# Kernel tuning notes

Measured on AMD Instinct MI355X. Metric: run time of the kernel, lower is better.

The kernel has to match this reference:

```python
import jax, jax.numpy as jnp
import numpy as np

B, N, D, H = 4, 16384, 64, 8
MIN_FREQ = 1.0 / 64.0
SCALE = 1.0
EPS = 1e-5


def layernorm(x):
    # LayerNorm over last (head-feature) dim, no affine, biased variance (torch default)
    m = jnp.mean(x, axis=-1, keepdims=True)
    v = jnp.mean(jnp.square(x - m), axis=-1, keepdims=True)
    return (x - m) * jax.lax.rsqrt(v + EPS)


def rope_freqs(pos):
    # pos: [b, n, 1] 1-D coordinates -> freqs [b, n, D]
    inv_freq = 1.0 / (10000.0 ** (jnp.arange(0, D, 2, dtype=jnp.float32) / D))  # [D/2]
    t = pos[..., 0] * (SCALE / MIN_FREQ)                                         # [b, n]
    f = t[..., None] * inv_freq                                                  # [b, n, D/2]
    return jnp.concatenate([f, f], axis=-1)                                      # [b, n, D]


def rotate_half(x):
    x1, x2 = jnp.split(x, 2, axis=-1)
    return jnp.concatenate([-x2, x1], axis=-1)


def apply_rope(x, freqs):
    # x: [b, h, n, d], freqs: [b, n, d]
    c = jnp.cos(freqs)[:, None]
    s = jnp.sin(freqs)[:, None]
    return x * c + rotate_half(x) * s


def setup_inputs() -> dict:
    key = jax.random.key(0)
    ks = jax.random.split(key, 6)
    gain = 1.0 / D
    return {
        "x": jax.random.normal(ks[0], (B, N, D), dtype=jnp.float32),
        "pos": jax.random.uniform(ks[1], (B, N, 1), dtype=jnp.float32),
        "Wq": jax.random.normal(ks[2], (D, D * H), dtype=jnp.float32) * gain,
        "Wk": jax.random.normal(ks[3], (D, D * H), dtype=jnp.float32) * gain,
        "Wv": jax.random.normal(ks[4], (D, D * H), dtype=jnp.float32) * gain,
        "Wo": jax.random.normal(ks[5], (D * H, D), dtype=jnp.float32) * gain,
    }


def reference(x, pos, Wq, Wk, Wv, Wo):
    b, n, _ = x.shape

    def proj(W):
        # [b, n, d] @ [d, h*d] -> [b, h, n, d]
        y = jnp.einsum("bnd,de->bne", x, W)
        return y.reshape(b, n, H, D).transpose(0, 2, 1, 3)

    q, k, v = proj(Wq), proj(Wk), proj(Wv)

    # galerkin: layernorm k and v (no mask path)
    k = layernorm(k)
    v = layernorm(v)

    # RoPE on q, k
    freqs = rope_freqs(pos)
    q = apply_rope(q, freqs)
    k = apply_rope(k, freqs)

    # linear attention: z = q @ (k^T v) / n
    kv = jnp.einsum("bhnd,bhne->bhde", k, v)          # [b, h, d, d]
    z = jnp.einsum("bhnd,bhde->bhne", q, kv) / n      # [b, h, n, d]
    z = z.transpose(0, 2, 1, 3).reshape(b, n, H * D)  # [b, n, h*d]

    return jnp.einsum("bne,ed->bnd", z, Wo)           # out_proj (dropout=0)
```

## Files before the change

kernel.cpp:

```cpp
#include <hip/hip_runtime.h>

#define B_ 4
#define N_ 16384
#define D_ 64
#define H_ 8
#define E_ 512
#define NCHUNK 16
#define NTILES (N_ / 64)

typedef __attribute__((ext_vector_type(8))) short short8;
typedef __attribute__((ext_vector_type(4))) float f32x4;
typedef __attribute__((ext_vector_type(2))) unsigned int uint32x2;

__device__ __forceinline__ unsigned short f2b(float f) {
    unsigned u = __float_as_uint(f);
    return (unsigned short)((u + 0x7fffu + ((u >> 16) & 1u)) >> 16);
}

__device__ __forceinline__ unsigned cvtpk(float a, float b) {
    unsigned r;
    asm("v_cvt_pk_bf16_f32 %0, %1, %2" : "=v"(r) : "v"(a), "v"(b));
    return r;
}

template<int CTRL>
__device__ __forceinline__ float dppadd(float x) {
    int y = __builtin_amdgcn_update_dpp(0, __float_as_int(x), CTRL, 0xF, 0xF, true);
    return x + __int_as_float(y);
}
__device__ __forceinline__ float rowsum16(float x) {
    x = dppadd<0xB1>(x);
    x = dppadd<0x4E>(x);
    x = dppadd<0x141>(x);
    x = dppadd<0x140>(x);
    return x;
}

__global__ __launch_bounds__(256) void k_prep(
    const float* __restrict__ x,
    const float* __restrict__ Wq, const float* __restrict__ Wk,
    const float* __restrict__ Wv,
    unsigned short* __restrict__ WqB, unsigned short* __restrict__ WkB,
    unsigned short* __restrict__ WvB,
    unsigned short* __restrict__ xblob)
{
    const int bid = blockIdx.x, tid = threadIdx.x;
    if (bid < 384) {
        int mat = bid >> 7, sub = bid & 127;
        const float* src = (mat == 0) ? Wq : (mat == 1) ? Wk : Wv;
        unsigned short* dst = (mat == 0) ? WqB : (mat == 1) ? WkB : WvB;
        int id = sub * 256 + tid;
        int kin = id >> 9, f = id & 511;
        int h = f >> 6, feat = f & 63;
        int nt = feat >> 4, cc = feat & 15;
        int half = kin >> 5, qd = (kin >> 3) & 3, e = kin & 7;
        dst[(size_t)h * 4096 + (((nt * 2 + half) * 64 + qd * 16 + cc) * 8) + e]
            = f2b(src[id]);
        return;
    }
    int idx = (bid - 384) * 256 + tid;
    int lane = idx & 63, fr = (idx >> 6) & 1, tb = (idx >> 7) & 1023, b = idx >> 17;
    int cc = lane & 15, qd = lane >> 4;
    const float* src = &x[((size_t)b * N_ + tb * 16 + cc) * 64 + fr * 32 + qd * 8];
    float4 v0 = *(const float4*)src;
    float4 v1 = *(const float4*)(src + 4);
    ushort4 u0, u1;
    u0.x = f2b(v0.x); u0.y = f2b(v0.y); u0.z = f2b(v0.z); u0.w = f2b(v0.w);
    u1.x = f2b(v1.x); u1.y = f2b(v1.y); u1.z = f2b(v1.z); u1.w = f2b(v1.w);
    *(ushort4*)&xblob[(size_t)idx * 8]     = u0;
    *(ushort4*)&xblob[(size_t)idx * 8 + 4] = u1;
}

__global__ __launch_bounds__(256, 2) void k_kv(
    const unsigned short* __restrict__ xblob,
    const float* __restrict__ pos,
    const unsigned short* __restrict__ WkB,
    const unsigned short* __restrict__ WvB,
    float* __restrict__ kv_part)
{
    const int b = blockIdx.z, h = blockIdx.y, chunk = blockIdx.x;
    const int tid  = threadIdx.x;
    const int lane = tid & 63;
    const int w    = tid >> 6;
    const int c    = lane & 15;
    const int quad = lane >> 4;
    const int m0   = w * 16;

    __shared__ unsigned short kbuf[2][64 * 72];
    __shared__ unsigned short vbuf[2][64 * 72];

    short8 WK[8], WV[8];
    {
        const unsigned short* wk0 = WkB + (size_t)h * 4096 + (size_t)lane * 8;
        const unsigned short* wv0 = WvB + (size_t)h * 4096 + (size_t)lane * 8;
        #pragma unroll
        for (int fr = 0; fr < 8; ++fr) WK[fr] = *(const short8*)&wk0[fr * 512];
        #pragma unroll
        for (int fr = 0; fr < 8; ++fr) WV[fr] = *(const short8*)&wv0[fr * 512];
    }
    __builtin_amdgcn_sched_barrier(0);

    const float invf_lo = exp2f(-0.4152410118609203f * (float)c);
    const float invf_hi = invf_lo * 0.01f;

    f32x4 akv[4];
    #pragma unroll
    for (int nt = 0; nt < 4; ++nt) akv[nt] = (f32x4){0.f, 0.f, 0.f, 0.f};

    short8 a0, a1;
    float tp[4];
    {
        int tb = chunk * 4 + w;
        const unsigned short* xb = xblob + (size_t)((b * 1024 + tb) * 2) * 512 + lane * 8;
        a0 = *(const short8*)&xb[0];
        a1 = *(const short8*)&xb[512];
        #pragma unroll
        for (int r = 0; r < 4; ++r)
            tp[r] = pos[(size_t)b * N_ + chunk * 64 + m0 + quad * 4 + r] * 64.0f;
    }

    int p = 0;
    for (int tile = chunk; tile < NTILES; tile += NCHUNK) {
        f32x4 ak[4], av[4];
        #pragma unroll
        for (int nt = 0; nt < 4; ++nt) {
            f32x4 z = {0.f, 0.f, 0.f, 0.f};
            z = __builtin_amdgcn_mfma_f32_16x16x32_bf16(a0, WK[nt * 2 + 0], z, 0, 0, 0);
            ak[nt] = __builtin_amdgcn_mfma_f32_16x16x32_bf16(a1, WK[nt * 2 + 1], z, 0, 0, 0);
            f32x4 y = {0.f, 0.f, 0.f, 0.f};
            y = __builtin_amdgcn_mfma_f32_16x16x32_bf16(a0, WV[nt * 2 + 0], y, 0, 0, 0);
            av[nt] = __builtin_amdgcn_mfma_f32_16x16x32_bf16(a1, WV[nt * 2 + 1], y, 0, 0, 0);
        }

        float cl[4], sl[4], ch[4], sh[4];
        #pragma unroll
        for (int r = 0; r < 4; ++r) {
            float al = tp[r] * invf_lo, ah = tp[r] * invf_hi;
            cl[r] = __cosf(al); sl[r] = __sinf(al);
            ch[r] = __cosf(ah); sh[r] = __sinf(ah);
        }

        const int tn = tile + NCHUNK;
        if (tn < NTILES) {
            int tb = tn * 4 + w;
            const unsigned short* xb = xblob + (size_t)((b * 1024 + tb) * 2) * 512 + lane * 8;
            a0 = *(const short8*)&xb[0];
            a1 = *(const short8*)&xb[512];
            #pragma unroll
            for (int r = 0; r < 4; ++r)
                tp[r] = pos[(size_t)b * N_ + tn * 64 + m0 + quad * 4 + r] * 64.0f;
        }
        __builtin_amdgcn_sched_barrier(0);

        #pragma unroll
        for (int r = 0; r < 4; ++r) {
            float sk  = ak[0][r] + ak[1][r] + ak[2][r] + ak[3][r];
            float sk2 = ak[0][r]*ak[0][r] + ak[1][r]*ak[1][r] + ak[2][r]*ak[2][r] + ak[3][r]*ak[3][r];
            float sv  = av[0][r] + av[1][r] + av[2][r] + av[3][r];
            float sv2 = av[0][r]*av[0][r] + av[1][r]*av[1][r] + av[2][r]*av[2][r] + av[3][r]*av[3][r];
            sk = rowsum16(sk); sk2 = rowsum16(sk2);
            sv = rowsum16(sv); sv2 = rowsum16(sv2);
            float mk = sk * (1.0f / 64.0f);
            float rk = rsqrtf(sk2 * (1.0f / 64.0f) - mk * mk + 1e-5f);
            float mv = sv * (1.0f / 64.0f);
            float rv = rsqrtf(sv2 * (1.0f / 64.0f) - mv * mv + 1e-5f);
            #pragma unroll
            for (int nt = 0; nt < 4; ++nt) {
                ak[nt][r] = (ak[nt][r] - mk) * rk;
                av[nt][r] = (av[nt][r] - mv) * rv;
            }
        }

        #pragma unroll
        for (int r = 0; r < 4; ++r) {
            float lo0 = ak[0][r], hi0 = ak[2][r];
            ak[0][r] = lo0 * cl[r] - hi0 * sl[r];
            ak[2][r] = hi0 * cl[r] + lo0 * sl[r];
            float lo1 = ak[1][r], hi1 = ak[3][r];
            ak[1][r] = lo1 * ch[r] - hi1 * sh[r];
            ak[3][r] = hi1 * ch[r] + lo1 * sh[r];
        }

        #pragma unroll
        for (int nt = 0; nt < 4; ++nt) {
            uint32x2 kk, vv;
            kk[0] = cvtpk(ak[nt][0], ak[nt][1]);
            kk[1] = cvtpk(ak[nt][2], ak[nt][3]);
            vv[0] = cvtpk(av[nt][0], av[nt][1]);
            vv[1] = cvtpk(av[nt][2], av[nt][3]);
            *(uint32x2*)&kbuf[p][(nt * 16 + c) * 72 + m0 + quad * 4] = kk;
            *(uint32x2*)&vbuf[p][(nt * 16 + c) * 72 + m0 + quad * 4] = vv;
        }
        __syncthreads();

        short8 ka0 = *(const short8*)&kbuf[p][(m0 + c) * 72 + quad * 8];
        short8 ka1 = *(const short8*)&kbuf[p][(m0 + c) * 72 + 32 + quad * 8];
        #pragma unroll
        for (int nt = 0; nt < 4; ++nt) {
            short8 vb0 = *(const short8*)&vbuf[p][(nt * 16 + c) * 72 + quad * 8];
            short8 vb1 = *(const short8*)&vbuf[p][(nt * 16 + c) * 72 + 32 + quad * 8];
            akv[nt] = __builtin_amdgcn_mfma_f32_16x16x32_bf16(ka0, vb0, akv[nt], 0, 0, 0);
            akv[nt] = __builtin_amdgcn_mfma_f32_16x16x32_bf16(ka1, vb1, akv[nt], 0, 0, 0);
        }
        p ^= 1;
    }

    float* dst = kv_part + ((size_t)(b * H_ + h) * NCHUNK + chunk) * 4096;
    #pragma unroll
    for (int nt = 0; nt < 4; ++nt)
        #pragma unroll
        for (int r = 0; r < 4; ++r)
            dst[(size_t)(16 * w + quad * 4 + r) * 64 + nt * 16 + c] = akv[nt][r];
}

__global__ __launch_bounds__(256) void k_m(
    const float* __restrict__ kv_part,
    const float* __restrict__ Wo,
    unsigned short* __restrict__ MTB)
{
    const int h = blockIdx.x, b = blockIdx.y;
    const int tid = threadIdx.x;
    __shared__ float kvs[64 * 65];
    __shared__ float wos[64 * 68];

    const float* src = kv_part + (size_t)(b * H_ + h) * NCHUNK * 4096;
    for (int i = tid; i < 4096; i += 256) {
        float s = 0.f;
        #pragma unroll
        for (int ch = 0; ch < NCHUNK; ++ch) s += src[ch * 4096 + i];
        kvs[(i >> 6) * 65 + (i & 63)] = s;
    }
    for (int i = tid; i < 1024; i += 256) {
        int dp = i >> 4, j4 = (i & 15) * 4;
        *(float4*)&wos[dp * 68 + j4] = *(const float4*)&Wo[(size_t)(h * 64 + dp) * 64 + j4];
    }
    __syncthreads();

    const int j0 = (tid & 15) * 4, d0 = (tid >> 4) * 4;
    float acc[4][4] = {{0.f}};
    #pragma unroll 4
    for (int dp = 0; dp < 64; ++dp) {
        float a_[4];
        #pragma unroll
        for (int i = 0; i < 4; ++i) a_[i] = kvs[(d0 + i) * 65 + dp];
        float4 w4 = *(const float4*)&wos[dp * 68 + j0];
        float w_[4] = {w4.x, w4.y, w4.z, w4.w};
        #pragma unroll
        for (int i = 0; i < 4; ++i)
            #pragma unroll
            for (int j = 0; j < 4; ++j)
                acc[i][j] += a_[i] * w_[j];
    }
    const float inv_n = 1.0f / (float)N_;
    unsigned short* dst = MTB + (size_t)(b * H_ + h) * 4096;
    #pragma unroll
    for (int i = 0; i < 4; ++i)
        #pragma unroll
        for (int j = 0; j < 4; ++j) {
            int d = d0 + i, jj = j0 + j;
            int nt = jj >> 4, cc = jj & 15;
            int half = d >> 5, qd = (d >> 3) & 3, e = d & 7;
            dst[(((nt * 2 + half) * 64 + qd * 16 + cc) * 8) + e] = f2b(acc[i][j] * inv_n);
        }
}

__global__ __launch_bounds__(256, 2) void k_out(
    const unsigned short* __restrict__ xblob,
    const float* __restrict__ pos,
    const unsigned short* __restrict__ WqB,
    const unsigned short* __restrict__ MTB,
    float* __restrict__ out)
{
    const int b = blockIdx.y;
    const int n0 = blockIdx.x * 64;
    const int tid  = threadIdx.x;
    const int lane = tid & 63;
    const int w    = tid >> 6;
    const int c    = lane & 15;
    const int quad = lane >> 4;
    const int m0   = w * 16;

    __shared__ unsigned short qbuf[64 * 72];

    const int tb = blockIdx.x * 4 + w;
    const unsigned short* xb = xblob + (size_t)((b * 1024 + tb) * 2) * 512 + lane * 8;
    short8 a0 = *(const short8*)&xb[0];
    short8 a1 = *(const short8*)&xb[512];

    const unsigned short* wq0 = WqB + (size_t)lane * 8;
    const unsigned short* mt0 = MTB + (size_t)(b * H_) * 4096 + (size_t)lane * 8;
    short8 W[8], Mt[8];
    #pragma unroll
    for (int fr = 0; fr < 8; ++fr) W[fr]  = *(const short8*)&wq0[fr * 512];
    #pragma unroll
    for (int fr = 0; fr < 8; ++fr) Mt[fr] = *(const short8*)&mt0[fr * 512];
    __builtin_amdgcn_sched_barrier(0);

    const float invf_lo = exp2f(-0.4152410118609203f * (float)c);
    const float invf_hi = invf_lo * 0.01f;
    float csl[4], snl[4], csh[4], snh[4];
    #pragma unroll
    for (int r = 0; r < 4; ++r) {
        float tpv = pos[(size_t)b * N_ + n0 + m0 + quad * 4 + r] * 64.0f;
        float al = tpv * invf_lo, ah = tpv * invf_hi;
        csl[r] = __cosf(al); snl[r] = __sinf(al);
        csh[r] = __cosf(ah); snh[r] = __sinf(ah);
    }

    f32x4 oacc[4];
    #pragma unroll
    for (int nt = 0; nt < 4; ++nt) oacc[nt] = (f32x4){0.f, 0.f, 0.f, 0.f};

    #pragma unroll
    for (int h = 0; h < H_; ++h) {
        f32x4 aq[4];
        #pragma unroll
        for (int nt = 0; nt < 4; ++nt) {
            f32x4 z = {0.f, 0.f, 0.f, 0.f};
            z = __builtin_amdgcn_mfma_f32_16x16x32_bf16(a0, W[nt * 2 + 0], z, 0, 0, 0);
            aq[nt] = __builtin_amdgcn_mfma_f32_16x16x32_bf16(a1, W[nt * 2 + 1], z, 0, 0, 0);
        }

        if (h < H_ - 1) {
            #pragma unroll
            for (int fr = 0; fr < 8; ++fr)
                W[fr] = *(const short8*)&wq0[(size_t)(h + 1) * 4096 + fr * 512];
        }
        __builtin_amdgcn_sched_barrier(0);

        #pragma unroll
        for (int r = 0; r < 4; ++r) {
            float lo0 = aq[0][r], hi0 = aq[2][r];
            aq[0][r] = lo0 * csl[r] - hi0 * snl[r];
            aq[2][r] = hi0 * csl[r] + lo0 * snl[r];
            float lo1 = aq[1][r], hi1 = aq[3][r];
            aq[1][r] = lo1 * csh[r] - hi1 * snh[r];
            aq[3][r] = hi1 * csh[r] + lo1 * snh[r];
        }

        #pragma unroll
        for (int nt = 0; nt < 4; ++nt) {
            unsigned q01 = cvtpk(aq[nt][0], aq[nt][1]);
            unsigned q23 = cvtpk(aq[nt][2], aq[nt][3]);
            int base = (m0 + quad * 4) * 72 + nt * 16 + c;
            qbuf[base]       = (unsigned short)q01;
            qbuf[base + 72]  = (unsigned short)(q01 >> 16);
            qbuf[base + 144] = (unsigned short)q23;
            qbuf[base + 216] = (unsigned short)(q23 >> 16);
        }

        short8 qa0 = *(const short8*)&qbuf[(m0 + c) * 72 + quad * 8];
        short8 qa1 = *(const short8*)&qbuf[(m0 + c) * 72 + 32 + quad * 8];
        #pragma unroll
        for (int nt = 0; nt < 4; ++nt) {
            oacc[nt] = __builtin_amdgcn_mfma_f32_16x16x32_bf16(qa0, Mt[nt * 2 + 0], oacc[nt], 0, 0, 0);
            oacc[nt] = __builtin_amdgcn_mfma_f32_16x16x32_bf16(qa1, Mt[nt * 2 + 1], oacc[nt], 0, 0, 0);
        }

        if (h < H_ - 1) {
            #pragma unroll
            for (int fr = 0; fr < 8; ++fr)
                Mt[fr] = *(const short8*)&mt0[(size_t)(h + 1) * 4096 + fr * 512];
        }
        __builtin_amdgcn_sched_barrier(0);
    }

    #pragma unroll
    for (int nt = 0; nt < 4; ++nt)
        #pragma unroll
        for (int r = 0; r < 4; ++r)
            out[(size_t)(b * N_ + n0 + m0 + quad * 4 + r) * 64 + nt * 16 + c] = oacc[nt][r];
}

extern "C" void kernel_launch(void* const* d_in, const int* in_sizes, int n_in,
                              void* d_out, int out_size, void* d_ws, size_t ws_size,
                              hipStream_t stream)
{
    const float* x   = (const float*)d_in[0];
    const float* pos = (const float*)d_in[1];
    const float* Wq  = (const float*)d_in[2];
    const float* Wk  = (const float*)d_in[3];
    const float* Wv  = (const float*)d_in[4];
    const float* Wo  = (const float*)d_in[5];
    float* out = (float*)d_out;

    char* ws = (char*)d_ws;
    float* kv_part        = (float*)ws;
    unsigned short* MTB   = (unsigned short*)(ws + 8388608);
    unsigned short* WqB   = (unsigned short*)(ws + 8650752);
    unsigned short* WkB   = (unsigned short*)(ws + 8716288);
    unsigned short* WvB   = (unsigned short*)(ws + 8781824);
    unsigned short* xblob = (unsigned short*)(ws + 8847360);

    k_prep<<<dim3(2432), 256, 0, stream>>>(x, Wq, Wk, Wv,
                                           WqB, WkB, WvB, xblob);
    k_kv  <<<dim3(NCHUNK, H_, B_), 256, 0, stream>>>(xblob, pos, WkB, WvB, kv_part);
    k_m   <<<dim3(H_, B_), 256, 0, stream>>>(kv_part, Wo, MTB);
    k_out <<<dim3(NTILES, B_), 256, 0, stream>>>(xblob, pos, WqB, MTB, out);
}
```

Before: 151.2 us.

## Double k_kv chunk count and process two 64-row tiles per k_out block

Raises k_kv parallelism from 16 to 32 chunks per (b,h) with a higher occupancy hint, and moves the workspace offsets to fit the larger partial buffer. k_out now handles 128 rows per block, so each Wq/Mt weight fragment loaded into registers is reused across two row tiles, halving the weight reloads and the block count. The cost is more register pressure in k_out, a larger kv_part reduction in k_m, and fewer k_out blocks to fill the GPU.

```diff
diff --git a/kernel.cpp b/kernel.cpp
--- a/kernel.cpp
+++ b/kernel.cpp
@@ -5,7 +5,7 @@
 #define D_ 64
 #define H_ 8
 #define E_ 512
-#define NCHUNK 16
+#define NCHUNK 32
 #define NTILES (N_ / 64)
 
 typedef __attribute__((ext_vector_type(8))) short short8;
@@ -71,7 +71,7 @@
     *(ushort4*)&xblob[(size_t)idx * 8 + 4] = u1;
 }
 
-__global__ __launch_bounds__(256, 2) void k_kv(
+__global__ __launch_bounds__(256, 4) void k_kv(
     const unsigned short* __restrict__ xblob,
     const float* __restrict__ pos,
     const unsigned short* __restrict__ WkB,
@@ -226,7 +226,7 @@
     const float* src = kv_part + (size_t)(b * H_ + h) * NCHUNK * 4096;
     for (int i = tid; i < 4096; i += 256) {
         float s = 0.f;
-        #pragma unroll
+        #pragma unroll 8
         for (int ch = 0; ch < NCHUNK; ++ch) s += src[ch * 4096 + i];
         kvs[(i >> 6) * 65 + (i & 63)] = s;
     }
@@ -272,7 +272,7 @@
     float* __restrict__ out)
 {
     const int b = blockIdx.y;
-    const int n0 = blockIdx.x * 64;
+    const int n0 = blockIdx.x * 128;
     const int tid  = threadIdx.x;
     const int lane = tid & 63;
     const int w    = tid >> 6;
@@ -280,12 +280,16 @@
     const int quad = lane >> 4;
     const int m0   = w * 16;
 
-    __shared__ unsigned short qbuf[64 * 72];
-
-    const int tb = blockIdx.x * 4 + w;
-    const unsigned short* xb = xblob + (size_t)((b * 1024 + tb) * 2) * 512 + lane * 8;
-    short8 a0 = *(const short8*)&xb[0];
-    short8 a1 = *(const short8*)&xb[512];
+    __shared__ unsigned short qbuf[128 * 72];
+
+    const int tbA = blockIdx.x * 8 + w;
+    const int tbB = blockIdx.x * 8 + 4 + w;
+    const unsigned short* xbA = xblob + (size_t)((b * 1024 + tbA) * 2) * 512 + lane * 8;
+    const unsigned short* xbB = xblob + (size_t)((b * 1024 + tbB) * 2) * 512 + lane * 8;
+    short8 aA0 = *(const short8*)&xbA[0];
+    short8 aA1 = *(const short8*)&xbA[512];
+    short8 aB0 = *(const short8*)&xbB[0];
+    short8 aB1 = *(const short8*)&xbB[512];
 
     const unsigned short* wq0 = WqB + (size_t)lane * 8;
     const unsigned short* mt0 = MTB + (size_t)(b * H_) * 4096 + (size_t)lane * 8;
@@ -298,27 +302,38 @@
 
     const float invf_lo = exp2f(-0.4152410118609203f * (float)c);
     const float invf_hi = invf_lo * 0.01f;
-    float csl[4], snl[4], csh[4], snh[4];
+    float cslA[4], snlA[4], cshA[4], snhA[4];
+    float cslB[4], snlB[4], cshB[4], snhB[4];
     #pragma unroll
     for (int r = 0; r < 4; ++r) {
-        float tpv = pos[(size_t)b * N_ + n0 + m0 + quad * 4 + r] * 64.0f;
-        float al = tpv * invf_lo, ah = tpv * invf_hi;
-        csl[r] = __cosf(al); snl[r] = __sinf(al);
-        csh[r] = __cosf(ah); snh[r] = __sinf(ah);
-    }
-
-    f32x4 oacc[4];
-    #pragma unroll
-    for (int nt = 0; nt < 4; ++nt) oacc[nt] = (f32x4){0.f, 0.f, 0.f, 0.f};
+        float tA = pos[(size_t)b * N_ + n0 + m0 + quad * 4 + r] * 64.0f;
+        float aAl = tA * invf_lo, aAh = tA * invf_hi;
+        cslA[r] = __cosf(aAl); snlA[r] = __sinf(aAl);
+        cshA[r] = __cosf(aAh); snhA[r] = __sinf(aAh);
+        float tB = pos[(size_t)b * N_ + n0 + 64 + m0 + quad * 4 + r] * 64.0f;
+        float aBl = tB * invf_lo, aBh = tB * invf_hi;
+        cslB[r] = __cosf(aBl); snlB[r] = __sinf(aBl);
+        cshB[r] = __cosf(aBh); snhB[r] = __sinf(aBh);
+    }
+
+    f32x4 oaccA[4], oaccB[4];
+    #pragma unroll
+    for (int nt = 0; nt < 4; ++nt) {
+        oaccA[nt] = (f32x4){0.f, 0.f, 0.f, 0.f};
+        oaccB[nt] = (f32x4){0.f, 0.f, 0.f, 0.f};
+    }
 
     #pragma unroll
     for (int h = 0; h < H_; ++h) {
-        f32x4 aq[4];
+        f32x4 aqA[4], aqB[4];
         #pragma unroll
         for (int nt = 0; nt < 4; ++nt) {
             f32x4 z = {0.f, 0.f, 0.f, 0.f};
-            z = __builtin_amdgcn_mfma_f32_16x16x32_bf16(a0, W[nt * 2 + 0], z, 0, 0, 0);
-            aq[nt] = __builtin_amdgcn_mfma_f32_16x16x32_bf16(a1, W[nt * 2 + 1], z, 0, 0, 0);
+            z = __builtin_amdgcn_mfma_f32_16x16x32_bf16(aA0, W[nt * 2 + 0], z, 0, 0, 0);
+            aqA[nt] = __builtin_amdgcn_mfma_f32_16x16x32_bf16(aA1, W[nt * 2 + 1], z, 0, 0, 0);
+            f32x4 y = {0.f, 0.f, 0.f, 0.f};
+            y = __builtin_amdgcn_mfma_f32_16x16x32_bf16(aB0, W[nt * 2 + 0], y, 0, 0, 0);
+            aqB[nt] = __builtin_amdgcn_mfma_f32_16x16x32_bf16(aB1, W[nt * 2 + 1], y, 0, 0, 0);
         }
 
         if (h < H_ - 1) {
@@ -330,31 +345,48 @@
 
         #pragma unroll
         for (int r = 0; r < 4; ++r) {
-            float lo0 = aq[0][r], hi0 = aq[2][r];
-            aq[0][r] = lo0 * csl[r] - hi0 * snl[r];
-            aq[2][r] = hi0 * csl[r] + lo0 * snl[r];
-            float lo1 = aq[1][r], hi1 = aq[3][r];
-            aq[1][r] = lo1 * csh[r] - hi1 * snh[r];
-            aq[3][r] = hi1 * csh[r] + lo1 * snh[r];
-        }
-
-        #pragma unroll
-        for (int nt = 0; nt < 4; ++nt) {
-            unsigned q01 = cvtpk(aq[nt][0], aq[nt][1]);
-            unsigned q23 = cvtpk(aq[nt][2], aq[nt][3]);
-            int base = (m0 + quad * 4) * 72 + nt * 16 + c;
-            qbuf[base]       = (unsigned short)q01;
-            qbuf[base + 72]  = (unsigned short)(q01 >> 16);
-            qbuf[base + 144] = (unsigned short)q23;
-            qbuf[base + 216] = (unsigned short)(q23 >> 16);
+            float lo0 = aqA[0][r], hi0 = aqA[2][r];
+            aqA[0][r] = lo0 * cslA[r] - hi0 * snlA[r];
+            aqA[2][r] = hi0 * cslA[r] + lo0 * snlA[r];
+            float lo1 = aqA[1][r], hi1 = aqA[3][r];
+            aqA[1][r] = lo1 * cshA[r] - hi1 * snhA[r];
+            aqA[3][r] = hi1 * cshA[r] + lo1 * snhA[r];
+            float lo2 = aqB[0][r], hi2 = aqB[2][r];
+            aqB[0][r] = lo2 * cslB[r] - hi2 * snlB[r];
+            aqB[2][r] = hi2 * cslB[r] + lo2 * snlB[r];
+            float lo3 = aqB[1][r], hi3 = aqB[3][r];
+            aqB[1][r] = lo3 * cshB[r] - hi3 * snhB[r];
+            aqB[3][r] = hi3 * cshB[r] + lo3 * snhB[r];
+        }
+
+        #pragma unroll
+        for (int nt = 0; nt < 4; ++nt) {
+            unsigned a01 = cvtpk(aqA[nt][0], aqA[nt][1]);
+            unsigned a23 = cvtpk(aqA[nt][2], aqA[nt][3]);
+            int baseA = (m0 + quad * 4) * 72 + nt * 16 + c;
+            qbuf[baseA]       = (unsigned short)a01;
+            qbuf[baseA + 72]  = (unsigned short)(a01 >> 16);
+            qbuf[baseA + 144] = (unsigned short)a23;
+            qbuf[baseA + 216] = (unsigned short)(a23 >> 16);
+            unsigned b01 = cvtpk(aqB[nt][0], aqB[nt][1]);
+            unsigned b23 = cvtpk(aqB[nt][2], aqB[nt][3]);
+            int baseB = (64 + m0 + quad * 4) * 72 + nt * 16 + c;
+            qbuf[baseB]       = (unsigned short)b01;
+            qbuf[baseB + 72]  = (unsigned short)(b01 >> 16);
+            qbuf[baseB + 144] = (unsigned short)b23;
+            qbuf[baseB + 216] = (unsigned short)(b23 >> 16);
         }
 
         short8 qa0 = *(const short8*)&qbuf[(m0 + c) * 72 + quad * 8];
         short8 qa1 = *(const short8*)&qbuf[(m0 + c) * 72 + 32 + quad * 8];
-        #pragma unroll
-        for (int nt = 0; nt < 4; ++nt) {
-            oacc[nt] = __builtin_amdgcn_mfma_f32_16x16x32_bf16(qa0, Mt[nt * 2 + 0], oacc[nt], 0, 0, 0);
-            oacc[nt] = __builtin_amdgcn_mfma_f32_16x16x32_bf16(qa1, Mt[nt * 2 + 1], oacc[nt], 0, 0, 0);
+        short8 qb0 = *(const short8*)&qbuf[(64 + m0 + c) * 72 + quad * 8];
+        short8 qb1 = *(const short8*)&qbuf[(64 + m0 + c) * 72 + 32 + quad * 8];
+        #pragma unroll
+        for (int nt = 0; nt < 4; ++nt) {
+            oaccA[nt] = __builtin_amdgcn_mfma_f32_16x16x32_bf16(qa0, Mt[nt * 2 + 0], oaccA[nt], 0, 0, 0);
+            oaccA[nt] = __builtin_amdgcn_mfma_f32_16x16x32_bf16(qa1, Mt[nt * 2 + 1], oaccA[nt], 0, 0, 0);
+            oaccB[nt] = __builtin_amdgcn_mfma_f32_16x16x32_bf16(qb0, Mt[nt * 2 + 0], oaccB[nt], 0, 0, 0);
+            oaccB[nt] = __builtin_amdgcn_mfma_f32_16x16x32_bf16(qb1, Mt[nt * 2 + 1], oaccB[nt], 0, 0, 0);
         }
 
         if (h < H_ - 1) {
@@ -368,8 +400,10 @@
     #pragma unroll
     for (int nt = 0; nt < 4; ++nt)
         #pragma unroll
-        for (int r = 0; r < 4; ++r)
-            out[(size_t)(b * N_ + n0 + m0 + quad * 4 + r) * 64 + nt * 16 + c] = oacc[nt][r];
+        for (int r = 0; r < 4; ++r) {
+            out[(size_t)(b * N_ + n0 + m0 + quad * 4 + r) * 64 + nt * 16 + c] = oaccA[nt][r];
+            out[(size_t)(b * N_ + n0 + 64 + m0 + quad * 4 + r) * 64 + nt * 16 + c] = oaccB[nt][r];
+        }
 }
 
 extern "C" void kernel_launch(void* const* d_in, const int* in_sizes, int n_in,
@@ -386,15 +420,15 @@
 
     char* ws = (char*)d_ws;
     float* kv_part        = (float*)ws;
-    unsigned short* MTB   = (unsigned short*)(ws + 8388608);
-    unsigned short* WqB   = (unsigned short*)(ws + 8650752);
-    unsigned short* WkB   = (unsigned short*)(ws + 8716288);
-    unsigned short* WvB   = (unsigned short*)(ws + 8781824);
-    unsigned short* xblob = (unsigned short*)(ws + 8847360);
+    unsigned short* MTB   = (unsigned short*)(ws + 16777216);
+    unsigned short* WqB   = (unsigned short*)(ws + 17039360);
+    unsigned short* WkB   = (unsigned short*)(ws + 17104896);
+    unsigned short* WvB   = (unsigned short*)(ws + 17170432);
+    unsigned short* xblob = (unsigned short*)(ws + 17235968);
 
     k_prep<<<dim3(2432), 256, 0, stream>>>(x, Wq, Wk, Wv,
                                            WqB, WkB, WvB, xblob);
     k_kv  <<<dim3(NCHUNK, H_, B_), 256, 0, stream>>>(xblob, pos, WkB, WvB, kv_part);
     k_m   <<<dim3(H_, B_), 256, 0, stream>>>(kv_part, Wo, MTB);
-    k_out <<<dim3(NTILES, B_), 256, 0, stream>>>(xblob, pos, WqB, MTB, out);
-}
+    k_out <<<dim3(NTILES / 2, B_), 256, 0, stream>>>(xblob, pos, WqB, MTB, out);
+}
```

Result: slower. 203.5 us (+34.6%).

## Stage Wk/Wv in LDS and double k_kv chunks for higher occupancy

Applied to the files above, without the earlier changes.

Moves the per-head Wk/Wv bf16 fragments from registers into shared memory, drops the double-buffered k/v staging for a single buffer plus an extra barrier, raises the launch-bounds occupancy hint to 4 blocks per CU, and doubles NCHUNK so k_kv launches twice as many blocks. The aim is to free VGPRs and fill the GPU better, since the original grid of 512 blocks is small. In exchange it adds LDS reads of the weights on every tile, one more barrier per tile, and a kv_part workspace twice as large for k_m to reduce.

```diff
diff --git a/kernel.cpp b/kernel.cpp
--- a/kernel.cpp
+++ b/kernel.cpp
@@ -5,7 +5,7 @@
 #define D_ 64
 #define H_ 8
 #define E_ 512
-#define NCHUNK 16
+#define NCHUNK 32
 #define NTILES (N_ / 64)
 
 typedef __attribute__((ext_vector_type(8))) short short8;
@@ -71,7 +71,7 @@
     *(ushort4*)&xblob[(size_t)idx * 8 + 4] = u1;
 }
 
-__global__ __launch_bounds__(256, 2) void k_kv(
+__global__ __launch_bounds__(256, 4) void k_kv(
     const unsigned short* __restrict__ xblob,
     const float* __restrict__ pos,
     const unsigned short* __restrict__ WkB,
@@ -86,19 +86,22 @@
     const int quad = lane >> 4;
     const int m0   = w * 16;
 
-    __shared__ unsigned short kbuf[2][64 * 72];
-    __shared__ unsigned short vbuf[2][64 * 72];
-
-    short8 WK[8], WV[8];
+    __shared__ unsigned short kbuf[64 * 72];
+    __shared__ unsigned short vbuf[64 * 72];
+    __shared__ unsigned short wkl[4096];
+    __shared__ unsigned short wvl[4096];
+
     {
-        const unsigned short* wk0 = WkB + (size_t)h * 4096 + (size_t)lane * 8;
-        const unsigned short* wv0 = WvB + (size_t)h * 4096 + (size_t)lane * 8;
-        #pragma unroll
-        for (int fr = 0; fr < 8; ++fr) WK[fr] = *(const short8*)&wk0[fr * 512];
-        #pragma unroll
-        for (int fr = 0; fr < 8; ++fr) WV[fr] = *(const short8*)&wv0[fr * 512];
-    }
-    __builtin_amdgcn_sched_barrier(0);
+        const float4* srcK = (const float4*)(WkB + (size_t)h * 4096);
+        const float4* srcV = (const float4*)(WvB + (size_t)h * 4096);
+        float4* dstK = (float4*)wkl;
+        float4* dstV = (float4*)wvl;
+        #pragma unroll
+        for (int i = 0; i < 2; ++i) {
+            dstK[tid + i * 256] = srcK[tid + i * 256];
+            dstV[tid + i * 256] = srcV[tid + i * 256];
+        }
+    }
 
     const float invf_lo = exp2f(-0.4152410118609203f * (float)c);
     const float invf_hi = invf_lo * 0.01f;
@@ -118,18 +121,22 @@
         for (int r = 0; r < 4; ++r)
             tp[r] = pos[(size_t)b * N_ + chunk * 64 + m0 + quad * 4 + r] * 64.0f;
     }
-
-    int p = 0;
+    __syncthreads();
+
     for (int tile = chunk; tile < NTILES; tile += NCHUNK) {
         f32x4 ak[4], av[4];
         #pragma unroll
         for (int nt = 0; nt < 4; ++nt) {
+            short8 bk0 = *(const short8*)&wkl[(nt * 2 + 0) * 512 + lane * 8];
+            short8 bk1 = *(const short8*)&wkl[(nt * 2 + 1) * 512 + lane * 8];
             f32x4 z = {0.f, 0.f, 0.f, 0.f};
-            z = __builtin_amdgcn_mfma_f32_16x16x32_bf16(a0, WK[nt * 2 + 0], z, 0, 0, 0);
-            ak[nt] = __builtin_amdgcn_mfma_f32_16x16x32_bf16(a1, WK[nt * 2 + 1], z, 0, 0, 0);
+            z = __builtin_amdgcn_mfma_f32_16x16x32_bf16(a0, bk0, z, 0, 0, 0);
+            ak[nt] = __builtin_amdgcn_mfma_f32_16x16x32_bf16(a1, bk1, z, 0, 0, 0);
+            short8 bv0 = *(const short8*)&wvl[(nt * 2 + 0) * 512 + lane * 8];
+            short8 bv1 = *(const short8*)&wvl[(nt * 2 + 1) * 512 + lane * 8];
             f32x4 y = {0.f, 0.f, 0.f, 0.f};
-            y = __builtin_amdgcn_mfma_f32_16x16x32_bf16(a0, WV[nt * 2 + 0], y, 0, 0, 0);
-            av[nt] = __builtin_amdgcn_mfma_f32_16x16x32_bf16(a1, WV[nt * 2 + 1], y, 0, 0, 0);
+            y = __builtin_amdgcn_mfma_f32_16x16x32_bf16(a0, bv0, y, 0, 0, 0);
+            av[nt] = __builtin_amdgcn_mfma_f32_16x16x32_bf16(a1, bv1, y, 0, 0, 0);
         }
 
         float cl[4], sl[4], ch[4], sh[4];
@@ -181,6 +188,8 @@
             ak[3][r] = hi1 * ch[r] + lo1 * sh[r];
         }
 
+        __syncthreads();
+
         #pragma unroll
         for (int nt = 0; nt < 4; ++nt) {
             uint32x2 kk, vv;
@@ -188,21 +197,20 @@
             kk[1] = cvtpk(ak[nt][2], ak[nt][3]);
             vv[0] = cvtpk(av[nt][0], av[nt][1]);
             vv[1] = cvtpk(av[nt][2], av[nt][3]);
-            *(uint32x2*)&kbuf[p][(nt * 16 + c) * 72 + m0 + quad * 4] = kk;
-            *(uint32x2*)&vbuf[p][(nt * 16 + c) * 72 + m0 + quad * 4] = vv;
+            *(uint32x2*)&kbuf[(nt * 16 + c) * 72 + m0 + quad * 4] = kk;
+            *(uint32x2*)&vbuf[(nt * 16 + c) * 72 + m0 + quad * 4] = vv;
         }
         __syncthreads();
 
-        short8 ka0 = *(const short8*)&kbuf[p][(m0 + c) * 72 + quad * 8];
-        short8 ka1 = *(const short8*)&kbuf[p][(m0 + c) * 72 + 32 + quad * 8];
-        #pragma unroll
-        for (int nt = 0; nt < 4; ++nt) {
-            short8 vb0 = *(const short8*)&vbuf[p][(nt * 16 + c) * 72 + quad * 8];
-            short8 vb1 = *(const short8*)&vbuf[p][(nt * 16 + c) * 72 + 32 + quad * 8];
+        short8 ka0 = *(const short8*)&kbuf[(m0 + c) * 72 + quad * 8];
+        short8 ka1 = *(const short8*)&kbuf[(m0 + c) * 72 + 32 + quad * 8];
+        #pragma unroll
+        for (int nt = 0; nt < 4; ++nt) {
+            short8 vb0 = *(const short8*)&vbuf[(nt * 16 + c) * 72 + quad * 8];
+            short8 vb1 = *(const short8*)&vbuf[(nt * 16 + c) * 72 + 32 + quad * 8];
             akv[nt] = __builtin_amdgcn_mfma_f32_16x16x32_bf16(ka0, vb0, akv[nt], 0, 0, 0);
             akv[nt] = __builtin_amdgcn_mfma_f32_16x16x32_bf16(ka1, vb1, akv[nt], 0, 0, 0);
         }
-        p ^= 1;
     }
 
     float* dst = kv_part + ((size_t)(b * H_ + h) * NCHUNK + chunk) * 4096;
@@ -226,7 +234,7 @@
     const float* src = kv_part + (size_t)(b * H_ + h) * NCHUNK * 4096;
     for (int i = tid; i < 4096; i += 256) {
         float s = 0.f;
-        #pragma unroll
+        #pragma unroll 8
         for (int ch = 0; ch < NCHUNK; ++ch) s += src[ch * 4096 + i];
         kvs[(i >> 6) * 65 + (i & 63)] = s;
     }
@@ -386,11 +394,11 @@
 
     char* ws = (char*)d_ws;
     float* kv_part        = (float*)ws;
-    unsigned short* MTB   = (unsigned short*)(ws + 8388608);
-    unsigned short* WqB   = (unsigned short*)(ws + 8650752);
-    unsigned short* WkB   = (unsigned short*)(ws + 8716288);
-    unsigned short* WvB   = (unsigned short*)(ws + 8781824);
-    unsigned short* xblob = (unsigned short*)(ws + 8847360);
+    unsigned short* MTB   = (unsigned short*)(ws + 16777216);
+    unsigned short* WqB   = (unsigned short*)(ws + 17039360);
+    unsigned short* WkB   = (unsigned short*)(ws + 17104896);
+    unsigned short* WvB   = (unsigned short*)(ws + 17170432);
+    unsigned short* xblob = (unsigned short*)(ws + 17235968);
 
     k_prep<<<dim3(2432), 256, 0, stream>>>(x, Wq, Wk, Wv,
                                            WqB, WkB, WvB, xblob);
```

New measurement: 162.1 us. 7.2% more time.
